# Kernel optimization log

Hardware: AMD Instinct MI355X
Metric: run time of the kernel (lower is better)

## Reference

```python
import jax, jax.numpy as jnp
import numpy as np

NLE_TERM_CO = 80
NUM_CHARS = 256
HID = 128


def setup_inputs() -> dict:
    key = jax.random.key(0)
    ks = jax.random.split(key, 9)
    B = 8192
    message = jax.random.randint(ks[0], (B, NLE_TERM_CO), 0, NUM_CHARS, dtype=jnp.int64)
    # Linear weights stored as (in, out); scaled like torch default init.
    s1 = 1.0 / np.sqrt(NLE_TERM_CO * NUM_CHARS)
    s2 = 1.0 / np.sqrt(HID)
    return {
        "message": message,
        "W1": jax.random.normal(ks[1], (NLE_TERM_CO * NUM_CHARS, HID), jnp.float32) * s1,
        "b1": jax.random.normal(ks[2], (HID,), jnp.float32) * s1,
        "W2": jax.random.normal(ks[3], (HID, HID), jnp.float32) * s2,
        "b2": jax.random.normal(ks[4], (HID,), jnp.float32) * s2,
        "W3": jax.random.normal(ks[5], (HID, HID), jnp.float32) * s2,
        "b3": jax.random.normal(ks[6], (HID,), jnp.float32) * s2,
        "W4": jax.random.normal(ks[7], (HID, HID), jnp.float32) * s2,
        "b4": jax.random.normal(ks[8], (HID,), jnp.float32) * s2,
    }


def reference(message, W1, b1, W2, b2, W3, b3, W4, b4):
    # one_hot(message) @ W1 == gather rows of W1 (viewed [pos, char, hid]) and sum over positions.
    # Exactly the same math (one-hot entries are exact 0.0/1.0 floats).
    W1r = W1.reshape(NLE_TERM_CO, NUM_CHARS, HID)
    pos = jnp.arange(NLE_TERM_CO)  # [80]
    h = W1r[pos, message]          # [B, 80, 128] gather per (position, char)
    h = jax.nn.elu(h.sum(axis=1) + b1)          # [B, 128]
    h = jax.nn.elu(h @ W2 + b2)
    h = jax.nn.elu(h @ W3 + b3)
    h = jax.nn.elu(h @ W4 + b4)
    return h
```

## Files before the change

### kernel.cpp

```cpp
#include <hip/hip_runtime.h>
#include <math.h>

#define HID  128
#define NPOS 80
#define XS   136

typedef float f4 __attribute__((ext_vector_type(4)));
typedef float f2 __attribute__((ext_vector_type(2)));
typedef unsigned int u32;
typedef u32 u32x4 __attribute__((ext_vector_type(4)));
typedef __attribute__((ext_vector_type(8))) short bf16x8;
typedef __attribute__((ext_vector_type(4))) float f32x4;

__device__ __forceinline__ float elu(float x) { return x > 0.f ? x : (expf(x) - 1.f); }
__device__ __forceinline__ unsigned short f2bf(float x) {
    u32 u = __float_as_uint(x);
    return (unsigned short)((u + 0x7fffu + ((u >> 16) & 1u)) >> 16);
}
__device__ __forceinline__ float bf2f(unsigned short h) { return __uint_as_float(((u32)h) << 16); }

__device__ __forceinline__ u32 f2e4m3(float x) {
    u32 u = __float_as_uint(x);
    u32 sign = (u >> 31) << 7;
    float a = fabsf(x);
    if (a >= 448.f) return sign | 0x7e;
    int e = (int)((u >> 23) & 0xff) - 127;
    if (e < -6) {
        int q = (int)rintf(a * 512.0f);
        if (q >= 8) return sign | 0x08;
        return sign | (u32)q;
    }
    u32 sig = (u & 0x7fffffu) | 0x800000u;
    u32 rs = sig + 0x7ffffu + ((sig >> 20) & 1u);
    if (rs >= 0x1000000u) { e += 1; rs >>= 1; }
    u32 m3 = (rs >> 20) & 7u;
    u32 enc = ((u32)(e + 7) << 3) | m3;
    if (enc >= 0x7fu) return sign | 0x7e;
    return sign | enc;
}

#if defined(__has_builtin)
#if __has_builtin(__builtin_amdgcn_cvt_pk_f32_fp8)
#define HW_FP8 1
#endif
#endif

#ifdef HW_FP8
__device__ __forceinline__ void dec4_acc(u32 v, f4* A) {
    f2 lo = __builtin_amdgcn_cvt_pk_f32_fp8((int)v, false);
    f2 hi = __builtin_amdgcn_cvt_pk_f32_fp8((int)v, true);
    (*A).x += lo.x; (*A).y += lo.y; (*A).z += hi.x; (*A).w += hi.y;
}
#else
__device__ __forceinline__ float dec1(u32 b) {
    int em = (int)(b & 0x7fu);
    int isn = (em >= 8) ? 1 : 0;
    int frac = (em & 7) | (isn << 3);
    int e2 = isn ? (em >> 3) : 1;
    float f = ldexpf((float)frac, e2 - 10);
    return (b & 0x80u) ? -f : f;
}
__device__ __forceinline__ void dec4_acc(u32 v, f4* A) {
    (*A).x += dec1(v & 0xff); (*A).y += dec1((v >> 8) & 0xff);
    (*A).z += dec1((v >> 16) & 0xff); (*A).w += dec1(v >> 24);
}
#endif

#define W1_BLOCKS 2560
#define TR_BLOCKS 24
__global__ __launch_bounds__(256) void prep(
    const float* __restrict__ W1, const float* __restrict__ W2,
    const float* __restrict__ W3, const float* __restrict__ W4,
    u32* __restrict__ W1f8,
    unsigned short* __restrict__ WtH, unsigned short* __restrict__ WtL)
{
    int b = blockIdx.x;
    if (b < W1_BLOCKS) {
        int i = b * 256 + threadIdx.x;
        f4 f = ((const f4*)W1)[i];
        u32 pk = f2e4m3(f.x * 64.f)
               | (f2e4m3(f.y * 64.f) << 8)
               | (f2e4m3(f.z * 64.f) << 16)
               | (f2e4m3(f.w * 64.f) << 24);
        W1f8[i] = pk;
    } else {
        int t = (b - W1_BLOCKS) * 256 + threadIdx.x;
        int lane = t & 63;
        int q = t >> 6;
        int kt = q & 3;  q >>= 2;
        int w  = q & 7;
        int L  = q >> 3;
        const float* W = (L == 0) ? W2 : (L == 1) ? W3 : W4;
        const int n    = w * 16 + (lane & 15);
        const int quad = lane >> 4;
        unsigned short hs[8], ls[8];
        #pragma unroll
        for (int j = 0; j < 8; ++j) {
            const int k = kt * 32 + quad * 8 + j;
            float v = W[k * HID + n];
            hs[j] = f2bf(v);
            ls[j] = f2bf(v - bf2f(hs[j]));
        }
        *(ushort4*)&WtH[t * 8]     = make_ushort4(hs[0], hs[1], hs[2], hs[3]);
        *(ushort4*)&WtH[t * 8 + 4] = make_ushort4(hs[4], hs[5], hs[6], hs[7]);
        *(ushort4*)&WtL[t * 8]     = make_ushort4(ls[0], ls[1], ls[2], ls[3]);
        *(ushort4*)&WtL[t * 8 + 4] = make_ushort4(ls[4], ls[5], ls[6], ls[7]);
    }
}

__global__ __launch_bounds__(512, 4) void main_k(
    const int* __restrict__ msg, const unsigned char* __restrict__ W1f8,
    const float* __restrict__ b1,
    const unsigned short* __restrict__ WtH, const unsigned short* __restrict__ WtL,
    const float* __restrict__ b2, const float* __restrict__ b3,
    const float* __restrict__ b4, float* __restrict__ out)
{
    const int tid = threadIdx.x, lane = tid & 63, w = tid >> 6;
    const int quad = lane >> 4, l15 = lane & 15;
    const int r0 = blockIdx.x * 16;

    __shared__ int smsg[16 * NPOS];
    __shared__ float P[4][16][HID];
    __shared__ unsigned short Xh[16 * XS];
    __shared__ unsigned short Xl[16 * XS];

    for (int k = tid; k < 16 * NPOS; k += 512)
        smsg[k] = msg[r0 * NPOS + k];
    __syncthreads();

    {
        const int qtr = w >> 1;
        const int rw  = ((w & 1) << 3) + (lane >> 3);
        const int co  = (lane & 7) << 4;
        const int* mr = &smsg[rw * NPOS];
        const int pbase = qtr * 20;
        f4 A0 = {0,0,0,0}, A1 = {0,0,0,0}, A2 = {0,0,0,0}, A3 = {0,0,0,0};
        #pragma unroll
        for (int h = 0; h < 2; ++h) {
            int c[10];
            #pragma unroll
            for (int u = 0; u < 10; ++u) c[u] = mr[pbase + h * 10 + u];
            u32x4 v[10];
            #pragma unroll
            for (int u = 0; u < 10; ++u)
                v[u] = *(const u32x4*)(W1f8 + (((pbase + h * 10 + u) << 15) + (c[u] << 7) + co));
            #pragma unroll
            for (int u = 0; u < 10; ++u) {
                dec4_acc(v[u].x, &A0); dec4_acc(v[u].y, &A1);
                dec4_acc(v[u].z, &A2); dec4_acc(v[u].w, &A3);
            }
        }
        float* Pp = &P[qtr][rw][(lane & 7) << 4];
        *(f4*)&Pp[0] = A0; *(f4*)&Pp[4] = A1; *(f4*)&Pp[8] = A2; *(f4*)&Pp[12] = A3;
    }
    __syncthreads();

    {
        const int m = tid >> 5, j0 = (tid & 31) << 2;
        f4 s = (*(const f4*)&P[0][m][j0] + *(const f4*)&P[1][m][j0]
              + *(const f4*)&P[2][m][j0] + *(const f4*)&P[3][m][j0]) * 0.015625f
              + *(const f4*)&b1[j0];
        float ys[4] = { elu(s.x), elu(s.y), elu(s.z), elu(s.w) };
        unsigned short hs[4], ls[4];
        #pragma unroll
        for (int u = 0; u < 4; ++u) {
            hs[u] = f2bf(ys[u]);
            ls[u] = f2bf(ys[u] - bf2f(hs[u]));
        }
        *(ushort4*)&Xh[m * XS + j0] = make_ushort4(hs[0], hs[1], hs[2], hs[3]);
        *(ushort4*)&Xl[m * XS + j0] = make_ushort4(ls[0], ls[1], ls[2], ls[3]);
    }
    __syncthreads();

    const float* bs[3] = { b2, b3, b4 };
    #pragma unroll 1
    for (int L = 0; L < 3; ++L) {
        bf16x8 Ah[4], Al[4];
        #pragma unroll
        for (int kt = 0; kt < 4; ++kt) {
            const int off = l15 * XS + kt * 32 + quad * 8;
            Ah[kt] = *(const bf16x8*)&Xh[off];
            Al[kt] = *(const bf16x8*)&Xl[off];
        }
        const unsigned short* WH = WtH + L * 16384;
        const unsigned short* WL = WtL + L * 16384;
        f32x4 acc = {0, 0, 0, 0};
        #pragma unroll
        for (int kt = 0; kt < 4; ++kt) {
            const int boff = (w * 4 + kt) * 512 + lane * 8;
            bf16x8 Bh = *(const bf16x8*)&WH[boff];
            bf16x8 Bl = *(const bf16x8*)&WL[boff];
            acc = __builtin_amdgcn_mfma_f32_16x16x32_bf16(Ah[kt], Bh, acc, 0, 0, 0);
            acc = __builtin_amdgcn_mfma_f32_16x16x32_bf16(Ah[kt], Bl, acc, 0, 0, 0);
            acc = __builtin_amdgcn_mfma_f32_16x16x32_bf16(Al[kt], Bh, acc, 0, 0, 0);
        }
        __syncthreads();

        const int n = w * 16 + l15;
        const float bias = bs[L][n];
        #pragma unroll
        for (int r = 0; r < 4; ++r) {
            const int mm = quad * 4 + r;
            const float y = elu(acc[r] + bias);
            if (L < 2) {
                unsigned short hi = f2bf(y);
                Xh[mm * XS + n] = hi;
                Xl[mm * XS + n] = f2bf(y - bf2f(hi));
            } else {
                out[(r0 + mm) * HID + n] = y;
            }
        }
        if (L < 2) __syncthreads();
    }
}

extern "C" void kernel_launch(void* const* d_in, const int* in_sizes, int n_in,
                              void* d_out, int out_size, void* d_ws, size_t ws_size,
                              hipStream_t stream) {
    const int*   msg = (const int*)  d_in[0];
    const float* W1  = (const float*)d_in[1];
    const float* b1  = (const float*)d_in[2];
    const float* W2  = (const float*)d_in[3];
    const float* b2  = (const float*)d_in[4];
    const float* W3  = (const float*)d_in[5];
    const float* b3  = (const float*)d_in[6];
    const float* W4  = (const float*)d_in[7];
    const float* b4  = (const float*)d_in[8];
    float* out = (float*)d_out;

    unsigned char*  W1f8 = (unsigned char*)d_ws;
    unsigned short* WtH  = (unsigned short*)(W1f8 + 2621440);
    unsigned short* WtL  = WtH + 49152;

    prep  <<<dim3(W1_BLOCKS + TR_BLOCKS), dim3(256), 0, stream>>>(W1, W2, W3, W4,
                                                                  (u32*)W1f8, WtH, WtL);
    main_k<<<dim3(512),                   dim3(512), 0, stream>>>(msg, W1f8, b1, WtH, WtL,
                                                                  b2, b3, b4, out);
}
```

Before: 95.42 us.

## Reduce W1 gather partials with wave shuffles instead of LDS and barrier

The gather now maps each half-wave to one row, with four position groups sharing a wave, and reduces the partial sums with xor shuffles. This replaces the LDS partial buffer P and one block barrier. Accumulation uses packed float2 adds from the fp8 conversion. The message loads and output stores become nontemporal. The change removes 32KB of LDS and a barrier, which may raise occupancy, at the cost of extra shuffle instructions and a select.

```diff
diff --git a/kernel.cpp b/kernel.cpp
--- a/kernel.cpp
+++ b/kernel.cpp
@@ -46,10 +46,9 @@
 #endif
 
 #ifdef HW_FP8
-__device__ __forceinline__ void dec4_acc(u32 v, f4* A) {
-    f2 lo = __builtin_amdgcn_cvt_pk_f32_fp8((int)v, false);
-    f2 hi = __builtin_amdgcn_cvt_pk_f32_fp8((int)v, true);
-    (*A).x += lo.x; (*A).y += lo.y; (*A).z += hi.x; (*A).w += hi.y;
+__device__ __forceinline__ void dec4_acc2(u32 v, f2& a0, f2& a1) {
+    a0 += __builtin_amdgcn_cvt_pk_f32_fp8((int)v, false);
+    a1 += __builtin_amdgcn_cvt_pk_f32_fp8((int)v, true);
 }
 #else
 __device__ __forceinline__ float dec1(u32 b) {
@@ -60,9 +59,9 @@
     float f = ldexpf((float)frac, e2 - 10);
     return (b & 0x80u) ? -f : f;
 }
-__device__ __forceinline__ void dec4_acc(u32 v, f4* A) {
-    (*A).x += dec1(v & 0xff); (*A).y += dec1((v >> 8) & 0xff);
-    (*A).z += dec1((v >> 16) & 0xff); (*A).w += dec1(v >> 24);
+__device__ __forceinline__ void dec4_acc2(u32 v, f2& a0, f2& a1) {
+    a0.x += dec1(v & 0xff);         a0.y += dec1((v >> 8) & 0xff);
+    a1.x += dec1((v >> 16) & 0xff); a1.y += dec1(v >> 24);
 }
 #endif
 
@@ -120,55 +119,65 @@
     const int r0 = blockIdx.x * 16;
 
     __shared__ int smsg[16 * NPOS];
-    __shared__ float P[4][16][HID];
     __shared__ unsigned short Xh[16 * XS];
     __shared__ unsigned short Xl[16 * XS];
 
     for (int k = tid; k < 16 * NPOS; k += 512)
-        smsg[k] = msg[r0 * NPOS + k];
+        smsg[k] = __builtin_nontemporal_load(&msg[r0 * NPOS + k]);
     __syncthreads();
 
     {
-        const int qtr = w >> 1;
-        const int rw  = ((w & 1) << 3) + (lane >> 3);
-        const int co  = (lane & 7) << 4;
-        const int* mr = &smsg[rw * NPOS];
-        const int pbase = qtr * 20;
-        f4 A0 = {0,0,0,0}, A1 = {0,0,0,0}, A2 = {0,0,0,0}, A3 = {0,0,0,0};
+        const int half = lane >> 5;
+        const int row  = (w << 1) | half;
+        const int l5   = lane & 31;
+        const int pg   = l5 >> 3;
+        const int colb = (l5 & 7) << 4;
+        const int* mr = &smsg[row * NPOS];
+        f2 A[8] = {};
         #pragma unroll
         for (int h = 0; h < 2; ++h) {
             int c[10];
             #pragma unroll
-            for (int u = 0; u < 10; ++u) c[u] = mr[pbase + h * 10 + u];
+            for (int u = 0; u < 10; ++u) c[u] = mr[pg + ((h * 10 + u) << 2)];
             u32x4 v[10];
             #pragma unroll
-            for (int u = 0; u < 10; ++u)
-                v[u] = *(const u32x4*)(W1f8 + (((pbase + h * 10 + u) << 15) + (c[u] << 7) + co));
+            for (int u = 0; u < 10; ++u) {
+                const int pos = pg + ((h * 10 + u) << 2);
+                v[u] = *(const u32x4*)(W1f8 + ((pos << 15) + (c[u] << 7) + colb));
+            }
             #pragma unroll
             for (int u = 0; u < 10; ++u) {
-                dec4_acc(v[u].x, &A0); dec4_acc(v[u].y, &A1);
-                dec4_acc(v[u].z, &A2); dec4_acc(v[u].w, &A3);
+                dec4_acc2(v[u].x, A[0], A[1]);
+                dec4_acc2(v[u].y, A[2], A[3]);
+                dec4_acc2(v[u].z, A[4], A[5]);
+                dec4_acc2(v[u].w, A[6], A[7]);
             }
         }
-        float* Pp = &P[qtr][rw][(lane & 7) << 4];
-        *(f4*)&Pp[0] = A0; *(f4*)&Pp[4] = A1; *(f4*)&Pp[8] = A2; *(f4*)&Pp[12] = A3;
-    }
-    __syncthreads();
-
-    {
-        const int m = tid >> 5, j0 = (tid & 31) << 2;
-        f4 s = (*(const f4*)&P[0][m][j0] + *(const f4*)&P[1][m][j0]
-              + *(const f4*)&P[2][m][j0] + *(const f4*)&P[3][m][j0]) * 0.015625f
-              + *(const f4*)&b1[j0];
-        float ys[4] = { elu(s.x), elu(s.y), elu(s.z), elu(s.w) };
-        unsigned short hs[4], ls[4];
-        #pragma unroll
-        for (int u = 0; u < 4; ++u) {
-            hs[u] = f2bf(ys[u]);
-            ls[u] = f2bf(ys[u] - bf2f(hs[u]));
-        }
-        *(ushort4*)&Xh[m * XS + j0] = make_ushort4(hs[0], hs[1], hs[2], hs[3]);
-        *(ushort4*)&Xl[m * XS + j0] = make_ushort4(ls[0], ls[1], ls[2], ls[3]);
+        #pragma unroll
+        for (int j = 0; j < 8; ++j) {
+            A[j].x += __shfl_xor(A[j].x, 8, 64);
+            A[j].y += __shfl_xor(A[j].y, 8, 64);
+        }
+        #pragma unroll
+        for (int j = 0; j < 8; ++j) {
+            A[j].x += __shfl_xor(A[j].x, 16, 64);
+            A[j].y += __shfl_xor(A[j].y, 16, 64);
+        }
+        f2 s0 = A[0], s1 = A[1];
+        if (pg == 1)      { s0 = A[2]; s1 = A[3]; }
+        else if (pg == 2) { s0 = A[4]; s1 = A[5]; }
+        else if (pg == 3) { s0 = A[6]; s1 = A[7]; }
+        const int colq = colb + (pg << 2);
+        const f4 bb = *(const f4*)&b1[colq];
+        const float y0 = elu(s0.x * 0.015625f + bb.x);
+        const float y1 = elu(s0.y * 0.015625f + bb.y);
+        const float y2 = elu(s1.x * 0.015625f + bb.z);
+        const float y3 = elu(s1.y * 0.015625f + bb.w);
+        const unsigned short h0 = f2bf(y0), h1 = f2bf(y1), h2 = f2bf(y2), h3 = f2bf(y3);
+        *(ushort4*)&Xh[row * XS + colq] = make_ushort4(h0, h1, h2, h3);
+        *(ushort4*)&Xl[row * XS + colq] = make_ushort4(
+            f2bf(y0 - bf2f(h0)), f2bf(y1 - bf2f(h1)),
+            f2bf(y2 - bf2f(h2)), f2bf(y3 - bf2f(h3)));
     }
     __syncthreads();
 
@@ -207,7 +216,7 @@
                 Xh[mm * XS + n] = hi;
                 Xl[mm * XS + n] = f2bf(y - bf2f(hi));
             } else {
-                out[(r0 + mm) * HID + n] = y;
+                __builtin_nontemporal_store(y, &out[(r0 + mm) * HID + n]);
             }
         }
         if (L < 2) __syncthreads();
```

Result: no change. 95.85 us (+0.5%).
